# Optimization experiments

Hardware: AMD Instinct MI355X
Metric: run time of the kernel (lower is better)

## Reference

```python
import jax, jax.numpy as jnp
import numpy as np
import math

NLAT, NLON, LMAX, MMAX = 128, 256, 50, 50
K = 3  # three_nn

# ---- precompute: Clenshaw-Curtis quadrature (torch_harmonics 'equiangular') ----
def _cc_nodes_weights(n):
    Nn = n - 1
    theta = np.pi * np.arange(n) / Nn
    v = np.zeros(n)
    for k in range(1, Nn // 2 + 1):
        b = 1.0 if 2 * k == Nn else 2.0
        v += b * np.cos(2 * k * theta) / (4 * k * k - 1)
    w = (2.0 / Nn) * (1.0 - v)
    w[0] *= 0.5
    w[-1] *= 0.5
    return np.cos(theta), w

# ---- precompute: orthonormal associated Legendre P_l^m(cos theta), csphase ----
def _legpoly(lmax, mmax, cost):
    sint = np.sqrt(np.clip(1.0 - cost ** 2, 0.0, None))
    p = np.zeros((mmax, lmax, cost.shape[0]))
    pmm = np.full(cost.shape[0], np.sqrt(1.0 / (4.0 * np.pi)))
    for m in range(mmax):
        if m > 0:
            pmm = -pmm * np.sqrt((2.0 * m + 1.0) / (2.0 * m)) * sint
        p[m, m] = pmm
        if m + 1 < lmax:
            p[m, m + 1] = np.sqrt(2.0 * m + 3.0) * cost * pmm
        for l in range(m + 2, lmax):
            a = np.sqrt((4.0 * l * l - 1.0) / (l * l - m * m))
            b = np.sqrt(((2.0 * l + 1.0) * (l - 1 + m) * (l - 1 - m)) / ((2.0 * l - 3.0) * (l * l - m * m)))
            p[m, l] = a * cost * p[m, l - 1] - b * p[m, l - 2]
    return p

_cost, _w = _cc_nodes_weights(NLAT)
_PCTW = jnp.asarray((_legpoly(LMAX, MMAX, _cost) * _w[None, None, :]).astype(np.float32))  # (mmax,lmax,nlat)

_gx, _gy = np.meshgrid(np.arange(NLAT), np.arange(-NLAT, NLAT), indexing='ij')
_GRID = jnp.asarray((np.stack([_gx.ravel(), _gy.ravel()], -1) / NLAT * np.pi).astype(np.float32))  # (M,2)

_RECTW = jnp.asarray(np.exp(-(LMAX - np.arange(1, LMAX + 1)) ** 2 / (2.0 * LMAX ** 2)).astype(np.float32))  # (lmax,)


def to_spherical(coords):
    # coords: (B,N,3) -> r:(B,N), sph:(B,N,2) = [arccos(x/r), azimuth in [0,2pi)]
    sq = coords ** 2
    pn = jnp.sqrt(jnp.flip(jnp.cumsum(jnp.flip(sq, -1), -1), -1))  # pn[...,i] = ||coords[...,i:]||
    r = pn[..., 0]
    phi = jnp.arccos(coords[..., :-2] / pn[..., :-2])
    a = jnp.arccos(coords[..., -2] / pn[..., -2])
    phi_final = a + (2.0 * math.pi - 2.0 * a) * (coords[..., -1] < 0)
    return r, jnp.concatenate([phi, phi_final[..., None]], axis=-1)


def interp_to_grid(coords):
    # spherical transform + 3-NN (squared dists) + distance-weighted interpolation onto the lat/lon grid
    r, sph = to_spherical(coords)
    sph = sph.at[..., 1].add(-math.pi)
    # brute-force pairwise squared distances grid(M,2) vs sph(B,N,2): (B,M,N)
    d2 = (jnp.sum(_GRID ** 2, -1)[None, :, None] + jnp.sum(sph ** 2, -1)[:, None, :]
          - 2.0 * jnp.einsum('md,bnd->bmn', _GRID, sph))
    _, idx = jax.lax.top_k(-jax.lax.stop_gradient(d2), K)  # (B,M,K), ascending distance
    sel = jax.vmap(lambda s, i: s[i])(sph, idx)            # (B,M,K,2)
    fsel = jax.vmap(lambda f, i: f[i])(r, idx)             # (B,M,K)
    dk = jnp.sum((_GRID[None, :, None, :] - sel) ** 2, -1)  # recompute selected sq-dists (differentiable)
    w = dk / jnp.sum(dk, -1, keepdims=True)                # weights = dist / sum(dist), as in source
    return jnp.sum(fsel * w, -1).reshape(-1, NLAT, NLON)


def sht_real(x):
    # RealSHT (equiangular, ortho): rfft(norm='forward')*2pi, then Legendre*quadrature einsum; real part only
    xf = jnp.fft.rfft(x, axis=-1)[..., :MMAX] * (2.0 * math.pi / NLON)
    return jnp.einsum('bkm,mlk->blm', jnp.real(xf).astype(jnp.float32), _PCTW)  # (B,lmax,mmax)


def setup_inputs() -> dict:
    key = jax.random.key(0)
    k1, k2 = jax.random.split(key)
    pred = jax.random.normal(k1, (2, 2048, 3), dtype=jnp.float32)
    target = jax.random.normal(k2, (2, 2048, 3), dtype=jnp.float32)
    return {"pred": pred, "target": target}


def reference(pred, target):
    pc = sht_real(interp_to_grid(pred))
    tc = sht_real(interp_to_grid(target))
    return jnp.mean(jnp.sum((pc - tc) ** 2 * _RECTW[None, :, None], axis=(1, 2)))
```

## Files before the change

kernel.cpp:

```cpp
#include <hip/hip_runtime.h>
#include <math.h>

#define PI_D 3.14159265358979323846
#define PIF  3.14159265358979323846f
#define NLAT 128
#define NLON 256
#define LMAX 50
#define MMAX 50
#define NPTS 2048
#define NBT 16
#define NBA 32
#define NBIN (NBT * NBA)
#define WBIN 0.19634954084936207f
#define INVW 5.092958178940651f
#define BIG 1e30f
#define KMASK 0xFFFFF800u

__device__ __forceinline__ void insert3(float kf, float& k0, float& k1, float& k2) {
    float n1 = __builtin_amdgcn_fmed3f(kf, k0, k1);
    float n2 = __builtin_amdgcn_fmed3f(kf, k1, k2);
    k0 = fminf(kf, k0);
    k1 = n1;
    k2 = n2;
}

__device__ __forceinline__ float mkkey(float gt, float gl, float2 tl, int idx) {
    float dt = gt - tl.x, dl = gl - tl.y;
    float d = fmaf(dt, dt, dl * dl);
    return __uint_as_float((__float_as_uint(d) & KMASK) | (unsigned)idx);
}

__global__ __launch_bounds__(256) void fused_main(
    const float* __restrict__ pred, const float* __restrict__ tgt,
    float* __restrict__ pctwT, float* __restrict__ fre, float* __restrict__ out) {

    __shared__ float2 s_btl[NPTS];
    __shared__ float  s_br[NPTS];
    __shared__ int    s_cnt[NBIN];
    __shared__ int    s_off[NBIN + 1];
    __shared__ float  ctab[NLON];
    __shared__ float  row[NLON];
    __shared__ float  part[200];

    int bid = blockIdx.x;
    int t = threadIdx.x;

    if (bid >= 512) {
        int k = bid - 512;
        if (k == 0 && t == 0) out[0] = 0.0f;
        if (t < MMAX) {
            int m = t;
            double theta = PI_D * (double)k / 127.0;
            double cost = cos(theta);
            double sint = sqrt(fmax(1.0 - cost * cost, 0.0));
            double c2 = cos(2.0 * theta);
            double two_c2 = 2.0 * c2;
            double cp = 1.0, cc = c2, v = 0.0;
            for (int tt = 1; tt <= 63; ++tt) {
                v += 2.0 * cc / (double)(4 * tt * tt - 1);
                double cn = two_c2 * cc - cp;
                cp = cc;
                cc = cn;
            }
            double w = (2.0 / 127.0) * (1.0 - v);
            if (k == 0 || k == 127) w *= 0.5;

            double pmm = sqrt(1.0 / (4.0 * PI_D));
            for (int i = 1; i <= m; ++i)
                pmm = -pmm * sqrt((2.0 * (double)i + 1.0) / (2.0 * (double)i)) * sint;

            float* o = pctwT + (size_t)k * MMAX + m;
            for (int l = 0; l < m; ++l) o[(size_t)l * NLAT * MMAX] = 0.0f;
            o[(size_t)m * NLAT * MMAX] = (float)(pmm * w);
            double plm2 = pmm, plm1 = 0.0;
            if (m + 1 < LMAX) {
                plm1 = sqrt(2.0 * (double)m + 3.0) * cost * pmm;
                o[(size_t)(m + 1) * NLAT * MMAX] = (float)(plm1 * w);
            }
            for (int l = m + 2; l < LMAX; ++l) {
                double ll = (double)l;
                double denom = ll * ll - (double)(m * m);
                double a = sqrt((4.0 * ll * ll - 1.0) / denom);
                double b = sqrt(((2.0 * ll + 1.0) * (double)(l - 1 + m) * (double)(l - 1 - m)) /
                                ((2.0 * ll - 3.0) * denom));
                double p = a * cost * plm1 - b * plm2;
                o[(size_t)l * NLAT * MMAX] = (float)(p * w);
                plm2 = plm1;
                plm1 = p;
            }
        }
        return;
    }

    int f = bid >> 7;
    int lat = bid & 127;
    const float* src = ((f < 2) ? pred : tgt) + (size_t)(f & 1) * NPTS * 3;

    s_cnt[t] = 0;
    s_cnt[t + 256] = 0;
    ctab[t] = (float)cos(2.0 * PI_D * (double)t / (double)NLON);
    __syncthreads();

    float pth[8], paz[8], pr[8];
    int pbin[8];
#pragma unroll
    for (int i = 0; i < 8; ++i) {
        int n = t + 256 * i;
        float x = src[3 * n], y = src[3 * n + 1], z = src[3 * n + 2];
        float s1 = z * z;
        float s2 = s1 + y * y;
        float s3 = s2 + x * x;
        float r = sqrtf(s3);
        float rho = sqrtf(s2);
        float th = acosf(x / r);
        float a = acosf(y / rho);
        float az = (z < 0.0f) ? (a + (2.0f * PIF - 2.0f * a)) : a;
        az -= PIF;
        int bt = min(max((int)(th * INVW), 0), NBT - 1);
        int ba = min(max((int)((az + PIF) * INVW), 0), NBA - 1);
        int b = bt * NBA + ba;
        pth[i] = th; paz[i] = az; pr[i] = r; pbin[i] = b;
        atomicAdd(&s_cnt[b], 1);
    }
    __syncthreads();

    if (t == 0) s_off[NBIN] = NPTS;
    if (t < 64) {
        int base = t * 8;
        int loc[8];
        int run = 0;
#pragma unroll
        for (int i = 0; i < 8; ++i) { loc[i] = run; run += s_cnt[base + i]; }
        int x = run;
#pragma unroll
        for (int d = 1; d < 64; d <<= 1) {
            int y = __shfl_up(x, d);
            if (t >= d) x += y;
        }
        int ex = x - run;
#pragma unroll
        for (int i = 0; i < 8; ++i) s_off[base + i] = ex + loc[i];
    }
    __syncthreads();
    s_cnt[t] = s_off[t];
    s_cnt[t + 256] = s_off[t + 256];
    __syncthreads();
#pragma unroll
    for (int i = 0; i < 8; ++i) {
        int pos = atomicAdd(&s_cnt[pbin[i]], 1);
        s_btl[pos] = make_float2(pth[i], paz[i]);
        s_br[pos] = pr[i];
    }
    __syncthreads();

    int j = t;
    float gt = (float)((double)lat * PI_D / 128.0);
    float gl = (float)(((double)j - 128.0) * PI_D / 128.0);
    float glp = gl + PIF;
    int bt0 = lat >> 3;
    int ba0 = j >> 3;

    float k0 = BIG, k1 = BIG, k2 = BIG;

    {
        int rtl = max(bt0 - 1, 0), rth = min(bt0 + 1, NBT - 1);
        int bal = max(ba0 - 1, 0), bah = min(ba0 + 1, NBA - 1);
        for (int bt = rtl; bt <= rth; ++bt) {
            int i = s_off[bt * NBA + bal];
            int i1 = s_off[bt * NBA + bah + 1];
            for (; i + 4 <= i1; i += 4) {
                float2 a0 = s_btl[i];
                float2 a1 = s_btl[i + 1];
                float2 a2 = s_btl[i + 2];
                float2 a3 = s_btl[i + 3];
                insert3(mkkey(gt, gl, a0, i), k0, k1, k2);
                insert3(mkkey(gt, gl, a1, i + 1), k0, k1, k2);
                insert3(mkkey(gt, gl, a2, i + 2), k0, k1, k2);
                insert3(mkkey(gt, gl, a3, i + 3), k0, k1, k2);
            }
            for (; i < i1; ++i)
                insert3(mkkey(gt, gl, s_btl[i], i), k0, k1, k2);
        }
    }

    bool done;
    {
        float safe = BIG;
        if (bt0 - 1 > 0)       safe = fminf(safe, gt - (float)(bt0 - 1) * WBIN);
        if (bt0 + 1 < NBT - 1) safe = fminf(safe, (float)(bt0 + 2) * WBIN - gt);
        if (ba0 - 1 > 0)       safe = fminf(safe, glp - (float)(ba0 - 1) * WBIN);
        if (ba0 + 1 < NBA - 1) safe = fminf(safe, (float)(ba0 + 2) * WBIN - glp);
        done = (k2 <= safe * safe);
    }

    for (int R = 2; R <= 31; ++R) {
        if (__all(done)) break;
        if (!done) {
            int btl = bt0 - R, bth = bt0 + R;
            int lo = max(btl, 0), hi = min(bth, NBT - 1);
            int bal = max(ba0 - R, 0), bah = min(ba0 + R, NBA - 1);
            for (int bt = lo; bt <= hi; ++bt) {
                if (bt == btl || bt == bth) {
                    int i0 = s_off[bt * NBA + bal];
                    int i1 = s_off[bt * NBA + bah + 1];
                    for (int i = i0; i < i1; ++i)
                        insert3(mkkey(gt, gl, s_btl[i], i), k0, k1, k2);
                } else {
                    if (ba0 - R >= 0) {
                        int b = bt * NBA + ba0 - R;
                        for (int i = s_off[b]; i < s_off[b + 1]; ++i)
                            insert3(mkkey(gt, gl, s_btl[i], i), k0, k1, k2);
                    }
                    if (ba0 + R <= NBA - 1) {
                        int b = bt * NBA + ba0 + R;
                        for (int i = s_off[b]; i < s_off[b + 1]; ++i)
                            insert3(mkkey(gt, gl, s_btl[i], i), k0, k1, k2);
                    }
                }
            }
            float safe = BIG;
            if (bt0 - R > 0)       safe = fminf(safe, gt - (float)(bt0 - R) * WBIN);
            if (bt0 + R < NBT - 1) safe = fminf(safe, (float)(bt0 + R + 1) * WBIN - gt);
            if (ba0 - R > 0)       safe = fminf(safe, glp - (float)(ba0 - R) * WBIN);
            if (ba0 + R < NBA - 1) safe = fminf(safe, (float)(ba0 + R + 1) * WBIN - glp);
            if (k2 <= safe * safe) done = true;
        }
    }

    {
        int i0 = __float_as_uint(k0) & 0x7FF;
        int i1 = __float_as_uint(k1) & 0x7FF;
        int i2 = __float_as_uint(k2) & 0x7FF;
        float2 p0 = s_btl[i0];
        float2 p1 = s_btl[i1];
        float2 p2 = s_btl[i2];
        float dt0 = gt - p0.x, dl0 = gl - p0.y;
        float dt1 = gt - p1.x, dl1 = gl - p1.y;
        float dt2 = gt - p2.x, dl2 = gl - p2.y;
        float d0 = fmaf(dt0, dt0, dl0 * dl0);
        float d1 = fmaf(dt1, dt1, dl1 * dl1);
        float d2 = fmaf(dt2, dt2, dl2 * dl2);
        float s = d0 + d1 + d2;
        row[j] = (d0 * s_br[i0] + d1 * s_br[i1] + d2 * s_br[i2]) / s;
    }
    __syncthreads();

    if (t < 200) {
        int mm = t >> 2, q = t & 3;
        int bs = q * 64;
        float acc = 0.0f;
        int p = (bs * mm) & (NLON - 1);
        for (int i = 0; i < 64; ++i) {
            acc += row[bs + i] * ctab[p];
            p = (p + mm) & (NLON - 1);
        }
        part[t] = acc;
    }
    __syncthreads();
    if (t < MMAX) {
        const float* pp = part + t * 4;
        fre[(f * NLAT + lat) * MMAX + t] =
            ((pp[0] + pp[1]) + (pp[2] + pp[3])) * (float)(2.0 * PI_D / (double)NLON);
    }
}

__global__ __launch_bounds__(256) void contract_loss(const float* __restrict__ fre,
                                                     const float* __restrict__ pctwT,
                                                     float* __restrict__ out) {
    int b = blockIdx.x / LMAX;
    int l = blockIdx.x % LMAX;
    int mm = threadIdx.x & 63;
    int kq = threadIdx.x >> 6;
    __shared__ float sp[4][64], st_[4][64];
    float pc = 0.0f, tc = 0.0f;
    if (mm < MMAX) {
        const float* pw = pctwT + ((size_t)l * NLAT + kq * 32) * MMAX + mm;
        const float* fp = fre + ((size_t)b * NLAT + kq * 32) * MMAX + mm;
        const float* ft = fre + ((size_t)(2 + b) * NLAT + kq * 32) * MMAX + mm;
#pragma unroll 8
        for (int k = 0; k < 32; ++k) {
            float w = pw[k * MMAX];
            pc += fp[k * MMAX] * w;
            tc += ft[k * MMAX] * w;
        }
    }
    sp[kq][mm] = pc;
    st_[kq][mm] = tc;
    __syncthreads();
    if (threadIdx.x < 64) {
        int m2 = threadIdx.x;
        float pcs = (sp[0][m2] + sp[1][m2]) + (sp[2][m2] + sp[3][m2]);
        float tcs = (st_[0][m2] + st_[1][m2]) + (st_[2][m2] + st_[3][m2]);
        float diff = pcs - tcs;
        double dl_ = (double)(49 - l);
        float rw = (float)exp(-(dl_ * dl_) / 5000.0);
        float contrib = (m2 < MMAX) ? diff * diff * rw * 0.5f : 0.0f;
        for (int off = 32; off > 0; off >>= 1) contrib += __shfl_down(contrib, off);
        if (m2 == 0) atomicAdd(out, contrib);
    }
}

extern "C" void kernel_launch(void* const* d_in, const int* in_sizes, int n_in,
                              void* d_out, int out_size, void* d_ws, size_t ws_size,
                              hipStream_t stream) {
    const float* pred = (const float*)d_in[0];
    const float* tgt = (const float*)d_in[1];
    float* ws = (float*)d_ws;

    float* pctwT = ws;
    float* fre   = ws + 320000;
    float* out = (float*)d_out;

    fused_main<<<640, 256, 0, stream>>>(pred, tgt, pctwT, fre, out);
    contract_loss<<<2 * LMAX, 256, 0, stream>>>(fre, pctwT, out);
}
```

Measured before the change: 86.30 us.

## Split point binning into a prep kernel and compute Legendre table in float

Previously each of the 512 latitude blocks recomputed the spherical transform, binning and counting sort of all 2048 points. A new prep kernel now does this once per field and writes the sorted points and bin offsets to workspace, and a separate knn kernel loads them into shared memory. The Legendre/quadrature table is now computed in float instead of double. The cosine contraction loop gets four independent accumulators. The cost is an extra kernel launch and a global round trip, and float Legendre recurrences up to degree 50 may lose accuracy.

```diff
diff --git a/kernel.cpp b/kernel.cpp
--- a/kernel.cpp
+++ b/kernel.cpp
@@ -30,75 +30,72 @@
     return __uint_as_float((__float_as_uint(d) & KMASK) | (unsigned)idx);
 }
 
-__global__ __launch_bounds__(256) void fused_main(
+__global__ __launch_bounds__(256) void prep_kernel(
     const float* __restrict__ pred, const float* __restrict__ tgt,
-    float* __restrict__ pctwT, float* __restrict__ fre, float* __restrict__ out) {
+    float2* __restrict__ gbtl, float* __restrict__ gbr, int* __restrict__ goff,
+    float* __restrict__ pctwT, float* __restrict__ out) {
 
     __shared__ float2 s_btl[NPTS];
     __shared__ float  s_br[NPTS];
     __shared__ int    s_cnt[NBIN];
     __shared__ int    s_off[NBIN + 1];
-    __shared__ float  ctab[NLON];
-    __shared__ float  row[NLON];
-    __shared__ float  part[200];
 
     int bid = blockIdx.x;
     int t = threadIdx.x;
 
-    if (bid >= 512) {
-        int k = bid - 512;
-        if (k == 0 && t == 0) out[0] = 0.0f;
-        if (t < MMAX) {
-            int m = t;
-            double theta = PI_D * (double)k / 127.0;
-            double cost = cos(theta);
-            double sint = sqrt(fmax(1.0 - cost * cost, 0.0));
-            double c2 = cos(2.0 * theta);
-            double two_c2 = 2.0 * c2;
-            double cp = 1.0, cc = c2, v = 0.0;
-            for (int tt = 1; tt <= 63; ++tt) {
-                v += 2.0 * cc / (double)(4 * tt * tt - 1);
-                double cn = two_c2 * cc - cp;
-                cp = cc;
-                cc = cn;
-            }
-            double w = (2.0 / 127.0) * (1.0 - v);
-            if (k == 0 || k == 127) w *= 0.5;
-
-            double pmm = sqrt(1.0 / (4.0 * PI_D));
-            for (int i = 1; i <= m; ++i)
-                pmm = -pmm * sqrt((2.0 * (double)i + 1.0) / (2.0 * (double)i)) * sint;
-
-            float* o = pctwT + (size_t)k * MMAX + m;
-            for (int l = 0; l < m; ++l) o[(size_t)l * NLAT * MMAX] = 0.0f;
-            o[(size_t)m * NLAT * MMAX] = (float)(pmm * w);
-            double plm2 = pmm, plm1 = 0.0;
-            if (m + 1 < LMAX) {
-                plm1 = sqrt(2.0 * (double)m + 3.0) * cost * pmm;
-                o[(size_t)(m + 1) * NLAT * MMAX] = (float)(plm1 * w);
-            }
-            for (int l = m + 2; l < LMAX; ++l) {
-                double ll = (double)l;
-                double denom = ll * ll - (double)(m * m);
-                double a = sqrt((4.0 * ll * ll - 1.0) / denom);
-                double b = sqrt(((2.0 * ll + 1.0) * (double)(l - 1 + m) * (double)(l - 1 - m)) /
-                                ((2.0 * ll - 3.0) * denom));
-                double p = a * cost * plm1 - b * plm2;
-                o[(size_t)l * NLAT * MMAX] = (float)(p * w);
-                plm2 = plm1;
-                plm1 = p;
-            }
+    if (bid >= 4) {
+        int k = bid - 4;
+        int m = t;
+        if (k == 0 && m == 0) out[0] = 0.0f;
+        if (m >= MMAX) return;
+
+        double thd = PI_D * (double)k / 127.0;
+        float cost = (float)cos(thd);
+        float sint = (float)sin(thd);
+
+        float c2 = (float)cos(2.0 * thd);
+        float two_c2 = 2.0f * c2;
+        float cp = 1.0f, cc = c2, v = 0.0f;
+        for (int tt = 1; tt <= 63; ++tt) {
+            v += 2.0f * cc / (float)(4 * tt * tt - 1);
+            float cn = two_c2 * cc - cp;
+            cp = cc;
+            cc = cn;
+        }
+        float w = (2.0f / 127.0f) * (1.0f - v);
+        if (k == 0 || k == 127) w *= 0.5f;
+
+        float pmm = sqrtf(1.0f / (4.0f * PIF));
+        for (int i = 1; i <= m; ++i)
+            pmm = -pmm * sqrtf((2.0f * (float)i + 1.0f) / (2.0f * (float)i)) * sint;
+
+        float* o = pctwT + (size_t)k * MMAX + m;
+        for (int l = 0; l < m; ++l) o[(size_t)l * NLAT * MMAX] = 0.0f;
+        o[(size_t)m * NLAT * MMAX] = pmm * w;
+        float plm2 = pmm, plm1 = 0.0f;
+        if (m + 1 < LMAX) {
+            plm1 = sqrtf(2.0f * (float)m + 3.0f) * cost * pmm;
+            o[(size_t)(m + 1) * NLAT * MMAX] = plm1 * w;
+        }
+        for (int l = m + 2; l < LMAX; ++l) {
+            float fl = (float)l;
+            float denom = fl * fl - (float)(m * m);
+            float a = sqrtf((4.0f * fl * fl - 1.0f) / denom);
+            float b = sqrtf(((2.0f * fl + 1.0f) * (float)(l - 1 + m) * (float)(l - 1 - m)) /
+                            ((2.0f * fl - 3.0f) * denom));
+            float p = a * cost * plm1 - b * plm2;
+            o[(size_t)l * NLAT * MMAX] = p * w;
+            plm2 = plm1;
+            plm1 = p;
         }
         return;
     }
 
-    int f = bid >> 7;
-    int lat = bid & 127;
+    int f = bid;
     const float* src = ((f < 2) ? pred : tgt) + (size_t)(f & 1) * NPTS * 3;
 
     s_cnt[t] = 0;
     s_cnt[t + 256] = 0;
-    ctab[t] = (float)cos(2.0 * PI_D * (double)t / (double)NLON);
     __syncthreads();
 
     float pth[8], paz[8], pr[8];
@@ -153,6 +150,42 @@
     }
     __syncthreads();
 
+    for (int n = t; n < NPTS; n += 256) {
+        gbtl[(size_t)f * NPTS + n] = s_btl[n];
+        gbr[(size_t)f * NPTS + n] = s_br[n];
+    }
+    for (int n = t; n <= NBIN; n += 256) goff[f * (NBIN + 1) + n] = s_off[n];
+}
+
+__global__ __launch_bounds__(256) void knn_kernel(
+    const float2* __restrict__ gbtl, const float* __restrict__ gbr,
+    const int* __restrict__ goff, float* __restrict__ fre) {
+
+    __shared__ float2 s_btl[NPTS];
+    __shared__ float  s_br[NPTS];
+    __shared__ int    s_off[NBIN + 1];
+    __shared__ float  ctab[NLON];
+    __shared__ float  row[NLON];
+    __shared__ float  part[200];
+
+    int bid = blockIdx.x;
+    int t = threadIdx.x;
+    int f = bid >> 7;
+    int lat = bid & 127;
+
+    {
+        const float4* b4 = (const float4*)(gbtl + (size_t)f * NPTS);
+        float4* s4 = (float4*)s_btl;
+        for (int i = t; i < NPTS / 2; i += 256) s4[i] = b4[i];
+        const float4* r4 = (const float4*)(gbr + (size_t)f * NPTS);
+        float4* sr4 = (float4*)s_br;
+        for (int i = t; i < NPTS / 4; i += 256) sr4[i] = r4[i];
+        const int* go = goff + f * (NBIN + 1);
+        for (int i = t; i <= NBIN; i += 256) s_off[i] = go[i];
+        ctab[t] = (float)cos(2.0 * PI_D * (double)t / (double)NLON);
+    }
+    __syncthreads();
+
     int j = t;
     float gt = (float)((double)lat * PI_D / 128.0);
     float gl = (float)(((double)j - 128.0) * PI_D / 128.0);
@@ -160,27 +193,27 @@
     int bt0 = lat >> 3;
     int ba0 = j >> 3;
 
+    auto scan_seg = [&](int i, int i1, float& q0, float& q1, float& q2) {
+        for (; i + 4 <= i1; i += 4) {
+            float2 a0 = s_btl[i];
+            float2 a1 = s_btl[i + 1];
+            float2 a2 = s_btl[i + 2];
+            float2 a3 = s_btl[i + 3];
+            insert3(mkkey(gt, gl, a0, i), q0, q1, q2);
+            insert3(mkkey(gt, gl, a1, i + 1), q0, q1, q2);
+            insert3(mkkey(gt, gl, a2, i + 2), q0, q1, q2);
+            insert3(mkkey(gt, gl, a3, i + 3), q0, q1, q2);
+        }
+        for (; i < i1; ++i)
+            insert3(mkkey(gt, gl, s_btl[i], i), q0, q1, q2);
+    };
+
     float k0 = BIG, k1 = BIG, k2 = BIG;
-
     {
         int rtl = max(bt0 - 1, 0), rth = min(bt0 + 1, NBT - 1);
         int bal = max(ba0 - 1, 0), bah = min(ba0 + 1, NBA - 1);
-        for (int bt = rtl; bt <= rth; ++bt) {
-            int i = s_off[bt * NBA + bal];
-            int i1 = s_off[bt * NBA + bah + 1];
-            for (; i + 4 <= i1; i += 4) {
-                float2 a0 = s_btl[i];
-                float2 a1 = s_btl[i + 1];
-                float2 a2 = s_btl[i + 2];
-                float2 a3 = s_btl[i + 3];
-                insert3(mkkey(gt, gl, a0, i), k0, k1, k2);
-                insert3(mkkey(gt, gl, a1, i + 1), k0, k1, k2);
-                insert3(mkkey(gt, gl, a2, i + 2), k0, k1, k2);
-                insert3(mkkey(gt, gl, a3, i + 3), k0, k1, k2);
-            }
-            for (; i < i1; ++i)
-                insert3(mkkey(gt, gl, s_btl[i], i), k0, k1, k2);
-        }
+        for (int bt = rtl; bt <= rth; ++bt)
+            scan_seg(s_off[bt * NBA + bal], s_off[bt * NBA + bah + 1], k0, k1, k2);
     }
 
     bool done;
@@ -201,20 +234,15 @@
             int bal = max(ba0 - R, 0), bah = min(ba0 + R, NBA - 1);
             for (int bt = lo; bt <= hi; ++bt) {
                 if (bt == btl || bt == bth) {
-                    int i0 = s_off[bt * NBA + bal];
-                    int i1 = s_off[bt * NBA + bah + 1];
-                    for (int i = i0; i < i1; ++i)
-                        insert3(mkkey(gt, gl, s_btl[i], i), k0, k1, k2);
+                    scan_seg(s_off[bt * NBA + bal], s_off[bt * NBA + bah + 1], k0, k1, k2);
                 } else {
                     if (ba0 - R >= 0) {
                         int b = bt * NBA + ba0 - R;
-                        for (int i = s_off[b]; i < s_off[b + 1]; ++i)
-                            insert3(mkkey(gt, gl, s_btl[i], i), k0, k1, k2);
+                        scan_seg(s_off[b], s_off[b + 1], k0, k1, k2);
                     }
                     if (ba0 + R <= NBA - 1) {
                         int b = bt * NBA + ba0 + R;
-                        for (int i = s_off[b]; i < s_off[b + 1]; ++i)
-                            insert3(mkkey(gt, gl, s_btl[i], i), k0, k1, k2);
+                        scan_seg(s_off[b], s_off[b + 1], k0, k1, k2);
                     }
                 }
             }
@@ -248,13 +276,20 @@
     if (t < 200) {
         int mm = t >> 2, q = t & 3;
         int bs = q * 64;
-        float acc = 0.0f;
+        float a0 = 0.0f, a1 = 0.0f, a2 = 0.0f, a3 = 0.0f;
         int p = (bs * mm) & (NLON - 1);
-        for (int i = 0; i < 64; ++i) {
-            acc += row[bs + i] * ctab[p];
-            p = (p + mm) & (NLON - 1);
-        }
-        part[t] = acc;
+        int st1 = mm & (NLON - 1);
+        int st2 = (2 * mm) & (NLON - 1);
+        int st3 = (3 * mm) & (NLON - 1);
+        int st4 = (4 * mm) & (NLON - 1);
+        for (int i = 0; i < 64; i += 4) {
+            a0 += row[bs + i] * ctab[p];
+            a1 += row[bs + i + 1] * ctab[(p + st1) & (NLON - 1)];
+            a2 += row[bs + i + 2] * ctab[(p + st2) & (NLON - 1)];
+            a3 += row[bs + i + 3] * ctab[(p + st3) & (NLON - 1)];
+            p = (p + st4) & (NLON - 1);
+        }
+        part[t] = (a0 + a1) + (a2 + a3);
     }
     __syncthreads();
     if (t < MMAX) {
@@ -307,10 +342,14 @@
     const float* tgt = (const float*)d_in[1];
     float* ws = (float*)d_ws;
 
-    float* pctwT = ws;
-    float* fre   = ws + 320000;
+    float*  pctwT = ws;
+    float*  fre   = ws + 320000;
+    float2* gbtl  = (float2*)(ws + 345600);
+    float*  gbr   = ws + 345600 + 16384;
+    int*    goff  = (int*)(ws + 345600 + 16384 + 8192);
     float* out = (float*)d_out;
 
-    fused_main<<<640, 256, 0, stream>>>(pred, tgt, pctwT, fre, out);
+    prep_kernel<<<132, 256, 0, stream>>>(pred, tgt, gbtl, gbr, goff, pctwT, out);
+    knn_kernel<<<512, 256, 0, stream>>>(gbtl, gbr, goff, fre);
     contract_loss<<<2 * LMAX, 256, 0, stream>>>(fre, pctwT, out);
 }
```

Result: slower. 91.29 us (+5.8%).
